# Kernel optimization log

Hardware: AMD Instinct MI355X
Metric: run time of the kernel (lower is better)

The kernel has to match this reference:

```python
import jax, jax.numpy as jnp
import numpy as np
import math

B, L, E, H, D = 2, 2048, 2048, 16, 128
LOGIT_SCALE_MAX = math.log(1.0 / 0.01)
EPS = 1e-6


def rms_norm(x, scale, eps=EPS):
    # UIOLayerNorm: no mean subtraction, no bias, fp32 internals
    x32 = x.astype(jnp.float32)
    ms = jnp.mean(x32 * x32, axis=-1, keepdims=True)
    return (scale * (x32 * jax.lax.rsqrt(ms + eps)).astype(x.dtype)).astype(x.dtype)


def apply_rotary(x, rope):
    # x: [b, l, h, d]; rope: [b, l, d] interpreted as (cos, sin) interleaved pairs
    b, l, h, d = x.shape
    xr = x.astype(jnp.float32).reshape(b, l, h, d // 2, 2)
    rc = rope.astype(jnp.float32).reshape(b, l, 1, d // 2, 2)
    out = jnp.stack(
        [xr[..., 0] * rc[..., 0] - xr[..., 1] * rc[..., 1],
         xr[..., 1] * rc[..., 0] + xr[..., 0] * rc[..., 1]], axis=-1)
    return out.reshape(b, l, h, d).astype(x.dtype)


def l2_normalize(x, eps=1e-12):
    # matches F.normalize(dim=-1): x / max(||x||, eps)
    n = jnp.sqrt(jnp.sum(x * x, axis=-1, keepdims=True))
    return x / jnp.maximum(n, eps)


def setup_inputs() -> dict:
    key = jax.random.key(0)
    ks = jax.random.split(key, 12)
    scale = 1.0 / math.sqrt(E)
    return {
        "inputs_q": jax.random.normal(ks[0], (B, L, E), jnp.float32),
        "inputs_kv": jax.random.normal(ks[1], (B, L, E), jnp.float32),
        "bias": jax.random.normal(ks[2], (1, 1, L, L), jnp.float32),
        "q_sinusoids": jax.random.uniform(ks[3], (B, L, D), jnp.float32, -1.0, 1.0),
        "k_sinusoids": jax.random.uniform(ks[4], (B, L, D), jnp.float32, -1.0, 1.0),
        "Wq": jax.random.normal(ks[5], (E, E), jnp.float32) * scale,
        "Wk": jax.random.normal(ks[6], (E, E), jnp.float32) * scale,
        "Wv": jax.random.normal(ks[7], (E, E), jnp.float32) * scale,
        "Wo": jax.random.normal(ks[8], (E, E), jnp.float32) * scale,
        "q_norm_scale": jnp.ones((D,), jnp.float32),
        "k_norm_scale": jnp.ones((D,), jnp.float32),
        "logit_scale": jnp.full((H,), math.log(10.0), jnp.float32),
    }


def reference(inputs_q, inputs_kv, bias, q_sinusoids, k_sinusoids,
              Wq, Wk, Wv, Wo, q_norm_scale, k_norm_scale, logit_scale):
    dtype = inputs_q.dtype
    b, ql, e = inputs_q.shape
    kl = inputs_kv.shape[1]
    # QKV projections (nn.Linear, no bias), split heads -> [b, len, h, d]
    q = (inputs_q @ Wq.T).reshape(b, ql, H, D)
    k = (inputs_kv @ Wk.T).reshape(b, kl, H, D)
    v = (inputs_kv @ Wv.T).reshape(b, kl, H, D)
    # qk_norm (UIO RMS norm over head_dim)
    q = rms_norm(q, q_norm_scale)
    k = rms_norm(k, k_norm_scale)
    # RoPE
    q = apply_rotary(q, q_sinusoids)
    k = apply_rotary(k, k_sinusoids)
    # float32_logits
    q32 = q.astype(jnp.float32)
    k32 = k.astype(jnp.float32)
    # scaled cosine attention: L2-normalize q,k; learned per-head logit scale
    scores = jnp.einsum("bqhd,bkhd->bhqk", l2_normalize(q32), l2_normalize(k32))
    ls = jnp.exp(jnp.minimum(logit_scale, LOGIT_SCALE_MAX))
    scores = scores * ls[None, :, None, None]
    scores = scores + bias.astype(scores.dtype)
    attn = jax.nn.softmax(scores, axis=-1).astype(dtype)
    out = jnp.einsum("bhqk,bkhd->bqhd", attn, v)
    out = out.reshape(b, ql, e)
    return out @ Wo.T
```

## Files before the change

### kernel.cpp

```cpp
#include <hip/hip_runtime.h>
#include <hip/hip_bf16.h>

#define B_ 2
#define L_ 2048
#define E_ 2048
#define H_ 16
#define D_ 128
#define M_ (B_*L_)
#define NT_ (E_/64)
#define LOGIT_SCALE_MAX_ 4.6051701859880914f
#define LOG2E_ 1.44269504088896f

typedef __bf16 bf16_t;
typedef __bf16 bf16x2 __attribute__((ext_vector_type(2)));
typedef __bf16 bf16x4 __attribute__((ext_vector_type(4)));
typedef __bf16 bf16x8 __attribute__((ext_vector_type(8)));
typedef float f32x4 __attribute__((ext_vector_type(4)));
typedef float f32x16 __attribute__((ext_vector_type(16)));

#define KS_BYTE(r, cb) ((r) * 256 + ((cb) ^ (((r) & 7) << 4)))
#define VS_BYTE(r, cb) (16384 + (r) * 128 + ((cb) ^ (((r) & 7) << 4)))

__global__ void cvt_f32_bf16_k(const float* __restrict__ s, bf16_t* __restrict__ d, int n4, float scale) {
    int i = blockIdx.x * 256 + threadIdx.x;
    if (i < n4) {
        float4 v = ((const float4*)s)[i];
        bf16x4 o = { (bf16_t)(v.x * scale), (bf16_t)(v.y * scale),
                     (bf16_t)(v.z * scale), (bf16_t)(v.w * scale) };
        ((bf16x4*)d)[i] = o;
    }
}

template<typename OutT, int GROUPS>
__global__ __launch_bounds__(256, 2) void gemm_pipe(
    const bf16_t* __restrict__ A0, const bf16_t* __restrict__ A1,
    const bf16_t* __restrict__ W0, OutT* __restrict__ C0) {
    __shared__ bf16_t As[2][128 * 64];
    __shared__ bf16_t Bs[2][128 * 64];
    const int tid = threadIdx.x;
    const int wid = tid >> 6, lane = tid & 63;
    int bid = blockIdx.x;
    {
        int cpx = (int)gridDim.x >> 3;
        bid = (bid & 7) * cpx + (bid >> 3);
    }
    const int g = bid >> 9;
    const int wg = bid & 511;
    const int bm = wg >> 4, bn = wg & 15;
    const long arow0 = (long)bm * 128;
    const long brow0 = (long)bn * 128;
    const int fr = lane & 15, fq = lane >> 4;
    const int srow = lane >> 3;
    const int scol = (lane & 7) * 8;
    const int wm = wid >> 1, wn = wid & 1;
    const bf16_t* Ab = ((GROUPS > 1 && g > 0) ? A1 : A0) + arow0 * E_;
    const bf16_t* Wb = W0 + (long)g * E_ * E_ + brow0 * E_;
    OutT* Cg = C0 + (long)g * M_ * E_;

    f32x4 acc[4][4] = {};

    auto STAGE = [&](int kt, int p) {
        #pragma unroll
        for (int q = 0; q < 4; ++q) {
            int row = wid * 32 + q * 8 + srow;
            __builtin_amdgcn_global_load_lds(
                (const __attribute__((address_space(1))) void*)(Ab + (long)row * E_ + kt + scol),
                (__attribute__((address_space(3))) void*)(&As[p][(wid * 32 + q * 8) * 64]), 16, 0, 0);
            __builtin_amdgcn_global_load_lds(
                (const __attribute__((address_space(1))) void*)(Wb + (long)row * E_ + kt + scol),
                (__attribute__((address_space(3))) void*)(&Bs[p][(wid * 32 + q * 8) * 64]), 16, 0, 0);
        }
    };

    STAGE(0, 0);
    int p = 0;
    bf16x8 a[2][4], b[2][4];
    for (int t = 0; t < NT_ - 1; ++t) {
        STAGE((t + 1) * 64, p ^ 1);
        asm volatile("s_waitcnt vmcnt(8)" ::: "memory");
        __builtin_amdgcn_s_barrier();
        __builtin_amdgcn_sched_barrier(0);
        #pragma unroll
        for (int kk = 0; kk < 2; ++kk) {
            #pragma unroll
            for (int mi = 0; mi < 4; ++mi)
                a[kk][mi] = *(const bf16x8*)&As[p][(wm * 64 + mi * 16 + fr) * 64 + kk * 32 + fq * 8];
            #pragma unroll
            for (int ni = 0; ni < 4; ++ni)
                b[kk][ni] = *(const bf16x8*)&Bs[p][(wn * 64 + ni * 16 + fr) * 64 + kk * 32 + fq * 8];
        }
        asm volatile("s_waitcnt lgkmcnt(0)" ::: "memory");
        __builtin_amdgcn_sched_barrier(0);
        __builtin_amdgcn_s_barrier();
        __builtin_amdgcn_s_setprio(1);
        #pragma unroll
        for (int kk = 0; kk < 2; ++kk)
            #pragma unroll
            for (int mi = 0; mi < 4; ++mi)
                #pragma unroll
                for (int ni = 0; ni < 4; ++ni)
                    acc[mi][ni] = __builtin_amdgcn_mfma_f32_16x16x32_bf16(a[kk][mi], b[kk][ni], acc[mi][ni], 0, 0, 0);
        __builtin_amdgcn_s_setprio(0);
        p ^= 1;
    }
    asm volatile("s_waitcnt vmcnt(0)" ::: "memory");
    __builtin_amdgcn_s_barrier();
    __builtin_amdgcn_sched_barrier(0);
    #pragma unroll
    for (int kk = 0; kk < 2; ++kk) {
        #pragma unroll
        for (int mi = 0; mi < 4; ++mi)
            a[kk][mi] = *(const bf16x8*)&As[p][(wm * 64 + mi * 16 + fr) * 64 + kk * 32 + fq * 8];
        #pragma unroll
        for (int ni = 0; ni < 4; ++ni)
            b[kk][ni] = *(const bf16x8*)&Bs[p][(wn * 64 + ni * 16 + fr) * 64 + kk * 32 + fq * 8];
        #pragma unroll
        for (int mi = 0; mi < 4; ++mi)
            #pragma unroll
            for (int ni = 0; ni < 4; ++ni)
                acc[mi][ni] = __builtin_amdgcn_mfma_f32_16x16x32_bf16(a[kk][mi], b[kk][ni], acc[mi][ni], 0, 0, 0);
    }
    #pragma unroll
    for (int mi = 0; mi < 4; ++mi) {
        #pragma unroll
        for (int i = 0; i < 4; ++i) {
            long row = arow0 + wm * 64 + mi * 16 + fq * 4 + i;
            OutT* crow = Cg + row * E_ + brow0 + wn * 64 + fr;
            #pragma unroll
            for (int ni = 0; ni < 4; ++ni)
                crow[ni * 16] = (OutT)acc[mi][ni][i];
        }
    }
}

__global__ __launch_bounds__(256) void postproc_k(
    const bf16_t* __restrict__ P, const float* __restrict__ sins,
    const float* __restrict__ nscale, bf16_t* __restrict__ out) {
    const int wid = threadIdx.x >> 6, lane = threadIdx.x & 63;
    const long g = (long)blockIdx.x * 4 + wid;
    const int h = (int)(g % H_);
    const long bl = g / H_;
    const int b = (int)(bl / L_), l = (int)(bl % L_);
    bf16x2 xv = *(const bf16x2*)(P + g * D_ + lane * 2);
    float x0 = (float)xv[0], x1 = (float)xv[1];
    float ss = x0 * x0 + x1 * x1;
    #pragma unroll
    for (int m = 1; m < 64; m <<= 1) ss += __shfl_xor(ss, m);
    float r = rsqrtf(ss * (1.0f / 128.0f) + 1e-6f);
    float y0 = x0 * r * nscale[lane * 2];
    float y1 = x1 * r * nscale[lane * 2 + 1];
    float2 cs = *(const float2*)(sins + bl * D_ + lane * 2);
    float z0 = y0 * cs.x - y1 * cs.y;
    float z1 = y1 * cs.x + y0 * cs.y;
    float n2 = z0 * z0 + z1 * z1;
    #pragma unroll
    for (int m = 1; m < 64; m <<= 1) n2 += __shfl_xor(n2, m);
    float inv = 1.0f / fmaxf(sqrtf(n2), 1e-12f);
    bf16x2 o = { (bf16_t)(z0 * inv), (bf16_t)(z1 * inv) };
    *(bf16x2*)(out + (((long)b * H_ + h) * L_ + l) * D_ + lane * 2) = o;
}

__global__ __launch_bounds__(256) void transpose_v_k(
    const bf16_t* __restrict__ Vp, bf16_t* __restrict__ Vt) {
    __shared__ bf16_t t[64 * 64];
    const int lb = blockIdx.x;
    const int db = blockIdx.y;
    const int bh = blockIdx.z;
    const int b = bh >> 4, h = bh & 15;
    const bf16_t* src = Vp + ((long)(b * L_ + lb * 64) * H_ + h) * D_ + db * 64;
    #pragma unroll
    for (int it = 0; it < 2; ++it) {
        int i = it * 256 + threadIdx.x;
        int r = i >> 3, c8 = i & 7;
        bf16x8 v = *(const bf16x8*)(src + (long)r * H_ * D_ + c8 * 8);
        *(bf16x8*)&t[r * 64 + (c8 ^ (r >> 3)) * 8] = v;
    }
    __syncthreads();
    bf16_t* dst = Vt + ((long)(b * H_ + h) * D_ + db * 64) * L_ + lb * 64;
    #pragma unroll
    for (int it = 0; it < 2; ++it) {
        int i = it * 256 + threadIdx.x;
        int d = i >> 3, l8 = i & 7;
        bf16x8 o;
        #pragma unroll
        for (int j = 0; j < 8; ++j) {
            int l = l8 * 8 + j;
            o[j] = t[l * 64 + ((d >> 3) ^ l8) * 8 + (d & 7)];
        }
        *(bf16x8*)(dst + (long)d * L_ + l8 * 8) = o;
    }
}

__global__ __launch_bounds__(256, 2) void attn_k(
    const bf16_t* __restrict__ Qn, const bf16_t* __restrict__ Kn,
    const bf16_t* __restrict__ Vt, const bf16_t* __restrict__ biasb,
    const float* __restrict__ lsg, bf16_t* __restrict__ AO) {
    __shared__ __align__(16) unsigned char smem[34816];
    const int tid = threadIdx.x;
    const int w = tid >> 6, lane = tid & 63;
    const int lane31 = lane & 31, hi = lane >> 5;
    const int qb = blockIdx.x, bh = blockIdx.y;
    const int b = bh >> 4, h = bh & 15;
    const float lsc2 = __expf(fminf(lsg[h], LOGIT_SCALE_MAX_)) * LOG2E_;
    const int qr0 = qb * 128;
    const int qloc = w * 32 + lane31;
    const bf16_t* qrow  = Qn + (((long)b * H_ + h) * L_ + qr0 + qloc) * D_;
    const bf16_t* kbase = Kn + (((long)b * H_ + h) * L_) * D_;
    const bf16_t* vtbase = Vt + ((long)(b * H_ + h) * D_) * L_;
    const bf16_t* brow  = biasb + (long)(qr0 + qloc) * L_;

    const int ksr = tid >> 4, ksc = (tid & 15) * 8;
    const int vsr = tid >> 3, vsc = (tid & 7) * 8;

    bf16x8 qreg[8];
    #pragma unroll
    for (int kk = 0; kk < 8; ++kk)
        qreg[kk] = *(const bf16x8*)(qrow + kk * 16 + 8 * hi);

    f32x16 oacc[4] = {};
    float l_ = 0.f;

    bf16x8 kreg[4], vreg[4];
    #pragma unroll
    for (int it = 0; it < 4; ++it) {
        kreg[it] = *(const bf16x8*)(kbase + (long)(it * 16 + ksr) * D_ + ksc);
        vreg[it] = *(const bf16x8*)(vtbase + (long)(it * 32 + vsr) * L_ + vsc);
    }

    for (int kt = 0; kt < L_; kt += 64) {
        __syncthreads();
        #pragma unroll
        for (int it = 0; it < 4; ++it) {
            *(bf16x8*)(smem + KS_BYTE(it * 16 + ksr, ksc * 2)) = kreg[it];
            *(bf16x8*)(smem + VS_BYTE(it * 32 + vsr, vsc * 2)) = vreg[it];
        }
        __syncthreads();
        const int ktn = (kt + 64 < L_) ? kt + 64 : 0;
        #pragma unroll
        for (int it = 0; it < 4; ++it) {
            kreg[it] = *(const bf16x8*)(kbase + (long)(ktn + it * 16 + ksr) * D_ + ksc);
            vreg[it] = *(const bf16x8*)(vtbase + (long)(it * 32 + vsr) * L_ + ktn + vsc);
        }
        bf16x4 bb[2][4];
        #pragma unroll
        for (int f = 0; f < 2; ++f)
            #pragma unroll
            for (int rr = 0; rr < 4; ++rr)
                bb[f][rr] = *(const bf16x4*)(brow + kt + f * 32 + rr * 8 + 4 * hi);
        f32x16 sacc[2] = {};
        __builtin_amdgcn_s_setprio(1);
        #pragma unroll
        for (int kk = 0; kk < 8; ++kk) {
            bf16x8 ak0 = *(const bf16x8*)(smem + KS_BYTE(lane31,      kk * 32 + 16 * hi));
            bf16x8 ak1 = *(const bf16x8*)(smem + KS_BYTE(32 + lane31, kk * 32 + 16 * hi));
            sacc[0] = __builtin_amdgcn_mfma_f32_32x32x16_bf16(ak0, qreg[kk], sacc[0], 0, 0, 0);
            sacc[1] = __builtin_amdgcn_mfma_f32_32x32x16_bf16(ak1, qreg[kk], sacc[1], 0, 0, 0);
        }
        __builtin_amdgcn_s_setprio(0);
        float ps = 0.f;
        unsigned int wv[2][4][2];
        #pragma unroll
        for (int f = 0; f < 2; ++f)
            #pragma unroll
            for (int rr = 0; rr < 4; ++rr)
                #pragma unroll
                for (int wi = 0; wi < 2; ++wi) {
                    float pa = __builtin_amdgcn_exp2f(sacc[f][rr * 4 + wi * 2]     * lsc2 + (float)bb[f][rr][wi * 2]);
                    float pc = __builtin_amdgcn_exp2f(sacc[f][rr * 4 + wi * 2 + 1] * lsc2 + (float)bb[f][rr][wi * 2 + 1]);
                    ps += pa + pc;
                    bf16x2 t = { (bf16_t)pa, (bf16_t)pc };
                    wv[f][rr][wi] = __builtin_bit_cast(unsigned int, t);
                }
        ps += __shfl_xor(ps, 32);
        l_ += ps;
        bf16x8 pb_[4];
        #pragma unroll
        for (int kk = 0; kk < 4; ++kk) {
            const int f = kk >> 1;
            const int a2 = (kk & 1) * 2;
            unsigned int A0 = wv[f][a2][0],     A1 = wv[f][a2][1];
            unsigned int B0 = wv[f][a2 + 1][0], B1 = wv[f][a2 + 1][1];
            unsigned int own0  = hi ? B0 : A0;
            unsigned int own1  = hi ? B1 : A1;
            unsigned int send0 = hi ? A0 : B0;
            unsigned int send1 = hi ? A1 : B1;
            unsigned int recv0 = __shfl_xor(send0, 32);
            unsigned int recv1 = __shfl_xor(send1, 32);
            uint4 uu;
            uu.x = hi ? recv0 : own0;
            uu.y = hi ? recv1 : own1;
            uu.z = hi ? own0  : recv0;
            uu.w = hi ? own1  : recv1;
            pb_[kk] = __builtin_bit_cast(bf16x8, uu);
        }
        __builtin_amdgcn_s_setprio(1);
        #pragma unroll
        for (int df = 0; df < 4; ++df)
            #pragma unroll
            for (int kk = 0; kk < 4; ++kk) {
                bf16x8 av = *(const bf16x8*)(smem + VS_BYTE(df * 32 + lane31, kk * 32 + 16 * hi));
                oacc[df] = __builtin_amdgcn_mfma_f32_32x32x16_bf16(av, pb_[kk], oacc[df], 0, 0, 0);
            }
        __builtin_amdgcn_s_setprio(0);
    }
    __syncthreads();
    float inv = 1.0f / l_;
    #pragma unroll
    for (int df = 0; df < 4; ++df)
        #pragma unroll
        for (int rg = 0; rg < 16; ++rg) {
            int d = df * 32 + (rg & 3) + 8 * (rg >> 2) + 4 * hi;
            *(bf16_t*)(smem + qloc * 264 + d * 2) = (bf16_t)(oacc[df][rg] * inv);
        }
    __syncthreads();
    #pragma unroll
    for (int it = 0; it < 8; ++it) {
        int idx = it * 256 + tid;
        int row = idx >> 4, c = idx & 15;
        bf16x8 v = *(const bf16x8*)(smem + row * 264 + c * 16);
        *(bf16x8*)(AO + ((long)b * L_ + qr0 + row) * E_ + h * D_ + c * 8) = v;
    }
}

extern "C" void kernel_launch(void* const* d_in, const int* in_sizes, int n_in,
                              void* d_out, int out_size, void* d_ws, size_t ws_size,
                              hipStream_t stream) {
    const float* inputs_q  = (const float*)d_in[0];
    const float* inputs_kv = (const float*)d_in[1];
    const float* bias      = (const float*)d_in[2];
    const float* q_sin     = (const float*)d_in[3];
    const float* k_sin     = (const float*)d_in[4];
    const float* Wq        = (const float*)d_in[5];
    const float* Wk        = (const float*)d_in[6];
    const float* Wv        = (const float*)d_in[7];
    const float* Wo        = (const float*)d_in[8];
    const float* qns       = (const float*)d_in[9];
    const float* kns       = (const float*)d_in[10];
    const float* lsg       = (const float*)d_in[11];

    bf16_t* ws = (bf16_t*)d_ws;
    const long NW = 4194304;
    const long NX = 8388608;
    bf16_t* Wq_b   = ws;
    bf16_t* Wk_b   = ws + NW;
    bf16_t* Wv_b   = ws + 2 * NW;
    bf16_t* Wo_b   = ws + 3 * NW;
    bf16_t* bias_b = ws + 4 * NW;
    bf16_t* Xq     = bias_b + NW;
    bf16_t* Xkv    = Xq + NX;
    bf16_t* Qp     = Xkv + NX;
    bf16_t* Kp     = Qp + NX;
    bf16_t* Vp     = Kp + NX;
    bf16_t* Qn = Xq;
    bf16_t* Kn = Xkv;
    bf16_t* AO = Qp;
    bf16_t* Vtr = Kp;
    if (ws_size < (size_t)(5 * NW + 5 * NX) * 2) return;

    auto cvt = [&](const float* s, bf16_t* d, long n, float scale) {
        int n4 = (int)(n / 4);
        cvt_f32_bf16_k<<<dim3((n4 + 255) / 256), dim3(256), 0, stream>>>(s, d, n4, scale);
    };
    cvt(Wq, Wq_b, NW, 1.0f);
    cvt(Wk, Wk_b, NW, 1.0f);
    cvt(Wv, Wv_b, NW, 1.0f);
    cvt(Wo, Wo_b, NW, 1.0f);
    cvt(bias, bias_b, NW, LOG2E_);
    cvt(inputs_q, Xq, NX, 1.0f);
    cvt(inputs_kv, Xkv, NX, 1.0f);

    gemm_pipe<bf16_t, 3><<<dim3(1536), dim3(256), 0, stream>>>(Xq, Xkv, Wq_b, Qp);

    postproc_k<<<dim3(16384), dim3(256), 0, stream>>>(Qp, q_sin, qns, Qn);
    postproc_k<<<dim3(16384), dim3(256), 0, stream>>>(Kp, k_sin, kns, Kn);

    transpose_v_k<<<dim3(L_ / 64, D_ / 64, B_ * H_), dim3(256), 0, stream>>>(Vp, Vtr);

    attn_k<<<dim3(L_ / 128, B_ * H_), dim3(256), 0, stream>>>(Qn, Kn, Vtr, bias_b, lsg, AO);

    gemm_pipe<float, 1><<<dim3(512), dim3(256), 0, stream>>>(AO, AO, Wo_b, (float*)d_out);
}
```

Measured before the change: 369.4 us.

## Swizzle GEMM LDS layout and merge conversion and postproc launches

Applies an XOR swizzle to the 16-byte column chunks that global_load_lds writes into the GEMM shared tiles, and matches it on the fragment reads, to reduce LDS bank conflicts. It also merges the seven fp32-to-bf16 conversion launches into one kernel over the contiguous workspace, and the Q and K postprocessing launches into one grid. This cuts launch overhead and tail effects, at the cost of per-thread branching on which source buffer to read.

```diff
diff --git a/kernel.cpp b/kernel.cpp
--- a/kernel.cpp
+++ b/kernel.cpp
@@ -21,14 +21,33 @@
 #define KS_BYTE(r, cb) ((r) * 256 + ((cb) ^ (((r) & 7) << 4)))
 #define VS_BYTE(r, cb) (16384 + (r) * 128 + ((cb) ^ (((r) & 7) << 4)))
 
-__global__ void cvt_f32_bf16_k(const float* __restrict__ s, bf16_t* __restrict__ d, int n4, float scale) {
-    int i = blockIdx.x * 256 + threadIdx.x;
-    if (i < n4) {
-        float4 v = ((const float4*)s)[i];
-        bf16x4 o = { (bf16_t)(v.x * scale), (bf16_t)(v.y * scale),
-                     (bf16_t)(v.z * scale), (bf16_t)(v.w * scale) };
-        ((bf16x4*)d)[i] = o;
-    }
+#define GEMM_FRAG_IDX(r, kk, fq) ((r) * 64 + ((((kk) * 4 + (fq)) ^ ((r) & 7)) * 8))
+
+#define NW_ 4194304L
+#define NX_ 8388608L
+__global__ void cvt_all_k(const float* __restrict__ xq, const float* __restrict__ xkv,
+                          const float* __restrict__ bias,
+                          const float* __restrict__ wq, const float* __restrict__ wk,
+                          const float* __restrict__ wv, const float* __restrict__ wo,
+                          bf16_t* __restrict__ ws) {
+    const long NW4 = NW_ / 4, NX4 = NX_ / 4;
+    long i4 = (long)blockIdx.x * 256 + threadIdx.x;
+    const float* src; long off; float scale = 1.0f;
+    if (i4 < 4 * NW4) {
+        long r = i4 / NW4;
+        src = (r == 0) ? wq : (r == 1) ? wk : (r == 2) ? wv : wo;
+        off = i4 - r * NW4;
+    } else if (i4 < 5 * NW4) {
+        src = bias; off = i4 - 4 * NW4; scale = LOG2E_;
+    } else if (i4 < 5 * NW4 + NX4) {
+        src = xq; off = i4 - 5 * NW4;
+    } else {
+        src = xkv; off = i4 - 5 * NW4 - NX4;
+    }
+    float4 v = ((const float4*)src)[off];
+    bf16x4 o = { (bf16_t)(v.x * scale), (bf16_t)(v.y * scale),
+                 (bf16_t)(v.z * scale), (bf16_t)(v.w * scale) };
+    ((bf16x4*)ws)[i4] = o;
 }
 
 template<typename OutT, int GROUPS>
@@ -51,7 +70,7 @@
     const long brow0 = (long)bn * 128;
     const int fr = lane & 15, fq = lane >> 4;
     const int srow = lane >> 3;
-    const int scol = (lane & 7) * 8;
+    const int scol = ((lane & 7) ^ srow) * 8;
     const int wm = wid >> 1, wn = wid & 1;
     const bf16_t* Ab = ((GROUPS > 1 && g > 0) ? A1 : A0) + arow0 * E_;
     const bf16_t* Wb = W0 + (long)g * E_ * E_ + brow0 * E_;
@@ -84,10 +103,10 @@
         for (int kk = 0; kk < 2; ++kk) {
             #pragma unroll
             for (int mi = 0; mi < 4; ++mi)
-                a[kk][mi] = *(const bf16x8*)&As[p][(wm * 64 + mi * 16 + fr) * 64 + kk * 32 + fq * 8];
+                a[kk][mi] = *(const bf16x8*)&As[p][GEMM_FRAG_IDX(wm * 64 + mi * 16 + fr, kk, fq)];
             #pragma unroll
             for (int ni = 0; ni < 4; ++ni)
-                b[kk][ni] = *(const bf16x8*)&Bs[p][(wn * 64 + ni * 16 + fr) * 64 + kk * 32 + fq * 8];
+                b[kk][ni] = *(const bf16x8*)&Bs[p][GEMM_FRAG_IDX(wn * 64 + ni * 16 + fr, kk, fq)];
         }
         asm volatile("s_waitcnt lgkmcnt(0)" ::: "memory");
         __builtin_amdgcn_sched_barrier(0);
@@ -110,10 +129,10 @@
     for (int kk = 0; kk < 2; ++kk) {
         #pragma unroll
         for (int mi = 0; mi < 4; ++mi)
-            a[kk][mi] = *(const bf16x8*)&As[p][(wm * 64 + mi * 16 + fr) * 64 + kk * 32 + fq * 8];
+            a[kk][mi] = *(const bf16x8*)&As[p][GEMM_FRAG_IDX(wm * 64 + mi * 16 + fr, kk, fq)];
         #pragma unroll
         for (int ni = 0; ni < 4; ++ni)
-            b[kk][ni] = *(const bf16x8*)&Bs[p][(wn * 64 + ni * 16 + fr) * 64 + kk * 32 + fq * 8];
+            b[kk][ni] = *(const bf16x8*)&Bs[p][GEMM_FRAG_IDX(wn * 64 + ni * 16 + fr, kk, fq)];
         #pragma unroll
         for (int mi = 0; mi < 4; ++mi)
             #pragma unroll
@@ -134,10 +153,17 @@
 }
 
 __global__ __launch_bounds__(256) void postproc_k(
-    const bf16_t* __restrict__ P, const float* __restrict__ sins,
-    const float* __restrict__ nscale, bf16_t* __restrict__ out) {
+    const bf16_t* __restrict__ Pq, const bf16_t* __restrict__ Pk,
+    const float* __restrict__ qsins, const float* __restrict__ ksins,
+    const float* __restrict__ qnscale, const float* __restrict__ knscale,
+    bf16_t* __restrict__ outq, bf16_t* __restrict__ outk) {
     const int wid = threadIdx.x >> 6, lane = threadIdx.x & 63;
-    const long g = (long)blockIdx.x * 4 + wid;
+    const int half = blockIdx.x >> 14;
+    const long g = (long)(blockIdx.x & 16383) * 4 + wid;
+    const bf16_t* P = half ? Pk : Pq;
+    const float* sins = half ? ksins : qsins;
+    const float* nscale = half ? knscale : qnscale;
+    bf16_t* out = half ? outk : outq;
     const int h = (int)(g % H_);
     const long bl = g / H_;
     const int b = (int)(bl / L_), l = (int)(bl % L_);
@@ -339,11 +365,9 @@
     const float* lsg       = (const float*)d_in[11];
 
     bf16_t* ws = (bf16_t*)d_ws;
-    const long NW = 4194304;
-    const long NX = 8388608;
+    const long NW = NW_;
+    const long NX = NX_;
     bf16_t* Wq_b   = ws;
-    bf16_t* Wk_b   = ws + NW;
-    bf16_t* Wv_b   = ws + 2 * NW;
     bf16_t* Wo_b   = ws + 3 * NW;
     bf16_t* bias_b = ws + 4 * NW;
     bf16_t* Xq     = bias_b + NW;
@@ -357,22 +381,15 @@
     bf16_t* Vtr = Kp;
     if (ws_size < (size_t)(5 * NW + 5 * NX) * 2) return;
 
-    auto cvt = [&](const float* s, bf16_t* d, long n, float scale) {
-        int n4 = (int)(n / 4);
-        cvt_f32_bf16_k<<<dim3((n4 + 255) / 256), dim3(256), 0, stream>>>(s, d, n4, scale);
-    };
-    cvt(Wq, Wq_b, NW, 1.0f);
-    cvt(Wk, Wk_b, NW, 1.0f);
-    cvt(Wv, Wv_b, NW, 1.0f);
-    cvt(Wo, Wo_b, NW, 1.0f);
-    cvt(bias, bias_b, NW, LOG2E_);
-    cvt(inputs_q, Xq, NX, 1.0f);
-    cvt(inputs_kv, Xkv, NX, 1.0f);
+    {
+        long n4 = (5 * NW + 2 * NX) / 4;
+        cvt_all_k<<<dim3((unsigned)(n4 / 256)), dim3(256), 0, stream>>>(
+            inputs_q, inputs_kv, bias, Wq, Wk, Wv, Wo, ws);
+    }
 
     gemm_pipe<bf16_t, 3><<<dim3(1536), dim3(256), 0, stream>>>(Xq, Xkv, Wq_b, Qp);
 
-    postproc_k<<<dim3(16384), dim3(256), 0, stream>>>(Qp, q_sin, qns, Qn);
-    postproc_k<<<dim3(16384), dim3(256), 0, stream>>>(Kp, k_sin, kns, Kn);
+    postproc_k<<<dim3(32768), dim3(256), 0, stream>>>(Qp, Kp, q_sin, k_sin, qns, kns, Qn, Kn);
 
     transpose_v_k<<<dim3(L_ / 64, D_ / 64, B_ * H_), dim3(256), 0, stream>>>(Vp, Vtr);
 
```

Result: faster. 319.4 us (-13.5%).
